# Kernel tuning notes

Measured on AMD Instinct MI355X. Metric: run time of the kernel, lower is better.

The kernel has to match this reference:

```python
import jax, jax.numpy as jnp
import numpy as np

D_IN = 1024
D_OUT = 1024
SEQ = 4096


def setup_inputs() -> dict:
    key = jax.random.key(0)
    kx, kq, kk, kv = jax.random.split(key, 4)
    s = 1.0 / np.sqrt(D_IN)
    return {
        "x": jax.random.normal(kx, (SEQ, D_IN), dtype=jnp.float32),
        # nn.Linear weights: shape [d_out, d_in], applied as x @ W.T
        "W_q": jax.random.uniform(kq, (D_OUT, D_IN), dtype=jnp.float32, minval=-s, maxval=s),
        "W_k": jax.random.uniform(kk, (D_OUT, D_IN), dtype=jnp.float32, minval=-s, maxval=s),
        "W_v": jax.random.uniform(kv, (D_OUT, D_IN), dtype=jnp.float32, minval=-s, maxval=s),
    }


def reference(x, W_q, W_k, W_v):
    # QKV projections (no bias)
    q = x @ W_q.T  # [N, d_out]
    k = x @ W_k.T
    v = x @ W_v.T
    d_k = k.shape[-1]
    scores = (q @ k.T) / jnp.sqrt(jnp.asarray(d_k, x.dtype))  # [N, N]
    attn = jax.nn.softmax(scores, axis=1)
    n = attn.shape[0]
    mask = jnp.tril(jnp.ones((n, n), dtype=attn.dtype))
    causal = attn * mask
    causal = causal / jnp.sum(causal, axis=1, keepdims=True)
    return causal @ v  # [N, d_out]
```

## Files before the change

kernel.cpp:

```cpp
#include <hip/hip_runtime.h>
#include <hip/hip_bf16.h>
#include <stdint.h>
#include <math.h>

#define SEQ 4096
#define DIM 1024

typedef __attribute__((ext_vector_type(8))) __bf16 bf16x8;
typedef __attribute__((ext_vector_type(4))) float f32x4;
typedef __attribute__((ext_vector_type(8))) unsigned short u16x8;

__device__ __forceinline__ unsigned short f2bf(float f) {
  unsigned int u = __float_as_uint(f);
  u = (u + 0x7FFFu + ((u >> 16) & 1u)) >> 16;
  return (unsigned short)u;
}

__device__ __forceinline__ int swz(int o) { return o ^ (((o >> 7) & 7) << 4); }

template <int N> __device__ __forceinline__ void wait_vm() {
  if constexpr (N == 0) asm volatile("s_waitcnt vmcnt(0)" ::: "memory");
  else if constexpr (N == 4) asm volatile("s_waitcnt vmcnt(4)" ::: "memory");
  else if constexpr (N == 6) asm volatile("s_waitcnt vmcnt(6)" ::: "memory");
  else if constexpr (N == 8) asm volatile("s_waitcnt vmcnt(8)" ::: "memory");
}

__global__ void __launch_bounds__(256) cvt_all(const float* __restrict__ x,
                                               const float* __restrict__ wq,
                                               const float* __restrict__ wk,
                                               const float* __restrict__ wv,
                                               unsigned short* __restrict__ xb,
                                               unsigned short* __restrict__ wqk,
                                               unsigned short* __restrict__ wvb) {
  const int bid = blockIdx.x;
  const float* src;
  unsigned short* dst;
  size_t base;
  if (bid < 2048)      { src = x;  dst = xb;                base = (size_t)bid * 2048; }
  else if (bid < 2560) { src = wq; dst = wqk;               base = (size_t)(bid - 2048) * 2048; }
  else if (bid < 3072) { src = wk; dst = wqk + 1024 * 1024; base = (size_t)(bid - 2560) * 2048; }
  else                 { src = wv; dst = wvb;               base = (size_t)(bid - 3072) * 2048; }
  size_t i = base + (size_t)threadIdx.x * 8;
  float4 a = *reinterpret_cast<const float4*>(src + i);
  float4 b = *reinterpret_cast<const float4*>(src + i + 4);
  u16x8 o;
  o[0] = f2bf(a.x); o[1] = f2bf(a.y); o[2] = f2bf(a.z); o[3] = f2bf(a.w);
  o[4] = f2bf(b.x); o[5] = f2bf(b.y); o[6] = f2bf(b.z); o[7] = f2bf(b.w);
  *reinterpret_cast<u16x8*>(dst + i) = o;
}

__global__ void __launch_bounds__(256) proj_qk(const unsigned short* __restrict__ A,
                                               const unsigned short* __restrict__ B,
                                               unsigned short* __restrict__ C) {
  constexpr int lda = DIM, ldb = DIM, ldc = 2048;
  const int tr = blockIdx.x >> 4, tc = blockIdx.x & 15;

  __shared__ __align__(16) unsigned short As[2][128 * 64];
  __shared__ __align__(16) unsigned short Bs[2][128 * 64];

  const int tid = threadIdx.x;
  const int lane = tid & 63;
  const int wid = tid >> 6;
  const int wr = wid >> 1, wc = wid & 1;
  const int l15 = lane & 15;
  const int kq = lane >> 4;

  f32x4 acc[4][4];
  #pragma unroll
  for (int m = 0; m < 4; ++m)
    #pragma unroll
    for (int n = 0; n < 4; ++n)
      acc[m][n] = (f32x4){0.f, 0.f, 0.f, 0.f};

  const unsigned short* Abase = A + (size_t)tr * 128 * lda;
  const unsigned short* Bbase = B + (size_t)tc * 128 * ldb;

  auto stage = [&](int buf, int kt) {
    const int k0 = kt << 6;
    #pragma unroll
    for (int i = 0; i < 4; ++i) {
      const int o = (i * 256 + tid) * 16;
      const int cs = (swz(o) >> 4) & 7;
      const unsigned short* ga = Abase + (size_t)(o >> 7) * lda + k0 + cs * 8;
      const unsigned short* gb = Bbase + (size_t)(o >> 7) * ldb + k0 + cs * 8;
      __builtin_amdgcn_global_load_lds(
          (const __attribute__((address_space(1))) unsigned int*)ga,
          (__attribute__((address_space(3))) unsigned int*)((char*)&As[buf][0] + o), 16, 0, 0);
      __builtin_amdgcn_global_load_lds(
          (const __attribute__((address_space(1))) unsigned int*)gb,
          (__attribute__((address_space(3))) unsigned int*)((char*)&Bs[buf][0] + o), 16, 0, 0);
    }
  };

  stage(0, 0);
  int cur = 0;
  for (int kt = 0; kt < 16; ++kt) {
    if (kt + 1 < 16) { stage(cur ^ 1, kt + 1); wait_vm<8>(); }
    else wait_vm<0>();
    __builtin_amdgcn_s_barrier();

    bf16x8 af[4][2], bv[4][2];
    #pragma unroll
    for (int m = 0; m < 4; ++m)
      #pragma unroll
      for (int ks = 0; ks < 2; ++ks) {
        const int row = wr * 64 + m * 16 + l15;
        af[m][ks] = *reinterpret_cast<const bf16x8*>(
            (const char*)&As[cur][0] + swz(row * 128 + kq * 16 + ks * 64));
      }
    #pragma unroll
    for (int n = 0; n < 4; ++n)
      #pragma unroll
      for (int ks = 0; ks < 2; ++ks) {
        const int row = wc * 64 + n * 16 + l15;
        bv[n][ks] = *reinterpret_cast<const bf16x8*>(
            (const char*)&Bs[cur][0] + swz(row * 128 + kq * 16 + ks * 64));
      }
    #pragma unroll
    for (int m = 0; m < 4; ++m)
      #pragma unroll
      for (int n = 0; n < 4; ++n) {
        acc[m][n] = __builtin_amdgcn_mfma_f32_16x16x32_bf16(af[m][0], bv[n][0], acc[m][n], 0, 0, 0);
        acc[m][n] = __builtin_amdgcn_mfma_f32_16x16x32_bf16(af[m][1], bv[n][1], acc[m][n], 0, 0, 0);
      }
    __builtin_amdgcn_s_barrier();
    cur ^= 1;
  }

  const int rbase = tr * 128 + wr * 64 + kq * 4;
  const int cbase = tc * 128 + wc * 64 + l15;
  #pragma unroll
  for (int m = 0; m < 4; ++m)
    #pragma unroll
    for (int n = 0; n < 4; ++n)
      #pragma unroll
      for (int i = 0; i < 4; ++i)
        C[(size_t)(rbase + m * 16 + i) * ldc + cbase + n * 16] = f2bf(acc[m][n][i]);
}

__global__ void __launch_bounds__(512) qkt_vt(const unsigned short* __restrict__ Q,
                                              const unsigned short* __restrict__ K,
                                              unsigned short* __restrict__ S,
                                              const unsigned short* __restrict__ wvb,
                                              const unsigned short* __restrict__ xb,
                                              unsigned short* __restrict__ vt) {
  __shared__ __align__(16) unsigned short As[2][256 * 64];
  __shared__ __align__(16) unsigned short Bs[2][256 * 64];

  const int bid = ((blockIdx.x & 7) << 5) + (blockIdx.x >> 3);
  const int tid = threadIdx.x;
  const int lane = tid & 63;
  const int wid = tid >> 6;

  if (bid < 136) {
    int tr = (int)((sqrtf(8.0f * bid + 1.0f) - 1.0f) * 0.5f);
    while ((tr + 1) * (tr + 2) / 2 <= bid) ++tr;
    while (tr * (tr + 1) / 2 > bid) --tr;
    const int tc = bid - tr * (tr + 1) / 2;

    constexpr int LDA = 2 * DIM, LDC = SEQ;
    constexpr float SCALE = 0.03125f;
    const int wr = wid >> 2;
    const int wc = wid & 3;
    const int l15 = lane & 15;
    const int kq = lane >> 4;

    const unsigned short* Abase = Q + (size_t)tr * 256 * LDA;
    const unsigned short* Bbase = K + (size_t)tc * 256 * LDA;

    f32x4 acc[8][4];
    #pragma unroll
    for (int m = 0; m < 8; ++m)
      #pragma unroll
      for (int n = 0; n < 4; ++n)
        acc[m][n] = (f32x4){0.f, 0.f, 0.f, 0.f};

    auto stage_half = [&](int buf, int kt, int h) {
      const int k0 = kt << 6;
      const bool isB = (h < 2);
      unsigned short* lb = isB ? &Bs[buf][0] : &As[buf][0];
      const unsigned short* gb = isB ? Bbase : Abase;
      #pragma unroll
      for (int i = 0; i < 2; ++i) {
        const int ot = ((h & 1) << 14) + ((i * 512 + tid) << 4);
        const int row = ot >> 7;
        const int cs = (swz(ot) >> 4) & 7;
        const unsigned short* g = gb + (size_t)row * LDA + k0 + cs * 8;
        __builtin_amdgcn_global_load_lds(
            (const __attribute__((address_space(1))) unsigned int*)g,
            (__attribute__((address_space(3))) unsigned int*)((char*)lb + ot), 16, 0, 0);
      }
    };

    bf16x8 a[4][2], bn0[2][2], bn1[2][2];

    auto rdA = [&](int b, int mi) {
      #pragma unroll
      for (int f = 0; f < 4; ++f) {
        const int row = wr * 128 + mi * 64 + f * 16 + l15;
        #pragma unroll
        for (int ks = 0; ks < 2; ++ks)
          a[f][ks] = *reinterpret_cast<const bf16x8*>(
              (const char*)&As[b][0] + swz(row * 128 + kq * 16 + ks * 64));
      }
    };
    auto rdB = [&](bf16x8 (&dst)[2][2], int b, int n) {
      #pragma unroll
      for (int g = 0; g < 2; ++g) {
        const int row = wc * 64 + n * 32 + g * 16 + l15;
        #pragma unroll
        for (int ks = 0; ks < 2; ++ks)
          dst[g][ks] = *reinterpret_cast<const bf16x8*>(
              (const char*)&Bs[b][0] + swz(row * 128 + kq * 16 + ks * 64));
      }
    };
    auto mma = [&](int mi, int n, bf16x8 (&bb)[2][2]) {
      #pragma unroll
      for (int f = 0; f < 4; ++f)
        #pragma unroll
        for (int g = 0; g < 2; ++g) {
          acc[mi * 4 + f][n * 2 + g] =
              __builtin_amdgcn_mfma_f32_16x16x32_bf16(a[f][0], bb[g][0], acc[mi * 4 + f][n * 2 + g], 0, 0, 0);
          acc[mi * 4 + f][n * 2 + g] =
              __builtin_amdgcn_mfma_f32_16x16x32_bf16(a[f][1], bb[g][1], acc[mi * 4 + f][n * 2 + g], 0, 0, 0);
        }
    };

    stage_half(0, 0, 0); stage_half(0, 0, 1); stage_half(0, 0, 2); stage_half(0, 0, 3);
    stage_half(1, 1, 0); stage_half(1, 1, 1);
    wait_vm<4>();
    __builtin_amdgcn_s_barrier();

    #pragma unroll 1
    for (int kt = 0; kt < 16; ++kt) {
      const int b = kt & 1;
      const bool pf1 = (kt + 1 < 16);
      const bool pf2 = (kt + 2 < 16);
      rdA(b, 0);
      rdB(bn0, b, 0);
      if (pf1) stage_half(b ^ 1, kt + 1, 2);
      __builtin_amdgcn_s_setprio(1); mma(0, 0, bn0); __builtin_amdgcn_s_setprio(0);
      __builtin_amdgcn_s_barrier();
      rdB(bn1, b, 1);
      if (pf1) stage_half(b ^ 1, kt + 1, 3);
      __builtin_amdgcn_s_setprio(1); mma(0, 1, bn1); __builtin_amdgcn_s_setprio(0);
      __builtin_amdgcn_s_barrier();
      rdA(b, 1);
      if (pf2) stage_half(b, kt + 2, 0);
      __builtin_amdgcn_s_setprio(1); mma(1, 1, bn1); __builtin_amdgcn_s_setprio(0);
      __builtin_amdgcn_s_barrier();
      if (pf2) stage_half(b, kt + 2, 1);
      if (pf1) { if (pf2) wait_vm<4>(); else wait_vm<0>(); }
      __builtin_amdgcn_s_setprio(1); mma(1, 0, bn0); __builtin_amdgcn_s_setprio(0);
      __builtin_amdgcn_s_barrier();
    }

    const int rb = tr * 256 + wr * 128 + kq * 4;
    const int cb = tc * 256 + wc * 64 + l15;
    #pragma unroll
    for (int am = 0; am < 8; ++am)
      #pragma unroll
      for (int an = 0; an < 4; ++an)
        #pragma unroll
        for (int i = 0; i < 4; ++i)
          S[(size_t)(rb + am * 16 + i) * LDC + cb + an * 16] = f2bf(acc[am][an][i] * SCALE);
    return;
  }

  const int wr = wid >> 1;
  const int wc = wid & 1;
  const int l15 = lane & 15;
  const int kq = lane >> 4;
  unsigned short* A0 = &As[0][0];
  unsigned short* B0 = &Bs[0][0];

  for (int t = bid - 136; t < 256; t += 120) {
    const int tr = t >> 5, tc = t & 31;
    const unsigned short* Abase = wvb + (size_t)tr * 128 * DIM;
    const unsigned short* Bbase = xb + (size_t)tc * 128 * DIM;

    f32x4 acc[2][4];
    #pragma unroll
    for (int m = 0; m < 2; ++m)
      #pragma unroll
      for (int n = 0; n < 4; ++n)
        acc[m][n] = (f32x4){0.f, 0.f, 0.f, 0.f};

    auto stage = [&](int buf, int kt) {
      const int k0 = kt << 6;
      #pragma unroll
      for (int i = 0; i < 2; ++i) {
        const int o = (i * 512 + tid) * 16;
        const int cs = (swz(o) >> 4) & 7;
        const unsigned short* ga = Abase + (size_t)(o >> 7) * DIM + k0 + cs * 8;
        const unsigned short* gb = Bbase + (size_t)(o >> 7) * DIM + k0 + cs * 8;
        __builtin_amdgcn_global_load_lds(
            (const __attribute__((address_space(1))) unsigned int*)ga,
            (__attribute__((address_space(3))) unsigned int*)((char*)(A0 + buf * 128 * 64) + o), 16, 0, 0);
        __builtin_amdgcn_global_load_lds(
            (const __attribute__((address_space(1))) unsigned int*)gb,
            (__attribute__((address_space(3))) unsigned int*)((char*)(B0 + buf * 128 * 64) + o), 16, 0, 0);
      }
    };

    stage(0, 0);
    int cur = 0;
    for (int kt = 0; kt < 16; ++kt) {
      if (kt + 1 < 16) { stage(cur ^ 1, kt + 1); wait_vm<4>(); }
      else wait_vm<0>();
      __builtin_amdgcn_s_barrier();

      bf16x8 af[2][2], bv[4][2];
      #pragma unroll
      for (int m = 0; m < 2; ++m)
        #pragma unroll
        for (int ks = 0; ks < 2; ++ks) {
          const int row = wr * 32 + m * 16 + l15;
          af[m][ks] = *reinterpret_cast<const bf16x8*>(
              (const char*)(A0 + cur * 128 * 64) + swz(row * 128 + kq * 16 + ks * 64));
        }
      #pragma unroll
      for (int n = 0; n < 4; ++n)
        #pragma unroll
        for (int ks = 0; ks < 2; ++ks) {
          const int row = wc * 64 + n * 16 + l15;
          bv[n][ks] = *reinterpret_cast<const bf16x8*>(
              (const char*)(B0 + cur * 128 * 64) + swz(row * 128 + kq * 16 + ks * 64));
        }
      #pragma unroll
      for (int m = 0; m < 2; ++m)
        #pragma unroll
        for (int n = 0; n < 4; ++n) {
          acc[m][n] = __builtin_amdgcn_mfma_f32_16x16x32_bf16(af[m][0], bv[n][0], acc[m][n], 0, 0, 0);
          acc[m][n] = __builtin_amdgcn_mfma_f32_16x16x32_bf16(af[m][1], bv[n][1], acc[m][n], 0, 0, 0);
        }
      __builtin_amdgcn_s_barrier();
      cur ^= 1;
    }

    const int rbase = tr * 128 + wr * 32 + kq * 4;
    const int cbase = tc * 128 + wc * 64 + l15;
    #pragma unroll
    for (int m = 0; m < 2; ++m)
      #pragma unroll
      for (int n = 0; n < 4; ++n)
        #pragma unroll
        for (int i = 0; i < 4; ++i)
          vt[(size_t)(rbase + m * 16 + i) * SEQ + cbase + n * 16] = f2bf(acc[m][n][i]);
    __builtin_amdgcn_s_barrier();
  }
}

__global__ void __launch_bounds__(256) pv_kernel(const unsigned short* __restrict__ A,
                                                 const unsigned short* __restrict__ B,
                                                 float* __restrict__ C,
                                                 float* __restrict__ P1, float* __restrict__ P2,
                                                 float* __restrict__ P3) {
  constexpr int BM = 64;
  constexpr int lda = SEQ, ldb = SEQ, ldc = DIM;
  int tc = blockIdx.x, tr = blockIdx.y;
  const int s = blockIdx.z;
  const int ltiles = tr + 1;
  int kt0 = s * 16;
  if (kt0 >= ltiles) return;
  const int nt = min(ltiles, kt0 + 16) - kt0;

  __shared__ __align__(16) unsigned short As[2][BM * 64];
  __shared__ __align__(16) unsigned short Bs[2][128 * 64];

  const int tid = threadIdx.x;
  const int lane = tid & 63;
  const int wid = tid >> 6;
  const int wr = wid >> 1, wc = wid & 1;
  const int l15 = lane & 15;
  const int kq = lane >> 4;

  f32x4 acc[2][4];
  #pragma unroll
  for (int m = 0; m < 2; ++m)
    #pragma unroll
    for (int n = 0; n < 4; ++n)
      acc[m][n] = (f32x4){0.f, 0.f, 0.f, 0.f};

  const unsigned short* Abase = A + (size_t)tr * BM * lda;
  const unsigned short* Bbase = B + (size_t)tc * 128 * ldb;

  auto stage = [&](int buf, int ktabs) {
    const int k0 = ktabs << 6;
    #pragma unroll
    for (int i = 0; i < 2; ++i) {
      const int o = (i * 256 + tid) * 16;
      const int cs = (swz(o) >> 4) & 7;
      const unsigned short* g = Abase + (size_t)(o >> 7) * lda + k0 + cs * 8;
      __builtin_amdgcn_global_load_lds(
          (const __attribute__((address_space(1))) unsigned int*)g,
          (__attribute__((address_space(3))) unsigned int*)((char*)&As[buf][0] + o), 16, 0, 0);
    }
    #pragma unroll
    for (int i = 0; i < 4; ++i) {
      const int o = (i * 256 + tid) * 16;
      const int cs = (swz(o) >> 4) & 7;
      const unsigned short* g = Bbase + (size_t)(o >> 7) * ldb + k0 + cs * 8;
      __builtin_amdgcn_global_load_lds(
          (const __attribute__((address_space(1))) unsigned int*)g,
          (__attribute__((address_space(3))) unsigned int*)((char*)&Bs[buf][0] + o), 16, 0, 0);
    }
  };

  stage(0, kt0);
  int cur = 0;
  for (int kt = 0; kt < nt; ++kt) {
    if (kt + 1 < nt) { stage(cur ^ 1, kt0 + kt + 1); wait_vm<6>(); }
    else wait_vm<0>();
    __builtin_amdgcn_s_barrier();

    bf16x8 af[2][2], bv[4][2];
    #pragma unroll
    for (int m = 0; m < 2; ++m)
      #pragma unroll
      for (int ks = 0; ks < 2; ++ks) {
        const int row = wr * 32 + m * 16 + l15;
        af[m][ks] = *reinterpret_cast<const bf16x8*>(
            (const char*)&As[cur][0] + swz(row * 128 + kq * 16 + ks * 64));
      }
    #pragma unroll
    for (int n = 0; n < 4; ++n)
      #pragma unroll
      for (int ks = 0; ks < 2; ++ks) {
        const int row = wc * 64 + n * 16 + l15;
        bv[n][ks] = *reinterpret_cast<const bf16x8*>(
            (const char*)&Bs[cur][0] + swz(row * 128 + kq * 16 + ks * 64));
      }
    #pragma unroll
    for (int m = 0; m < 2; ++m)
      #pragma unroll
      for (int n = 0; n < 4; ++n) {
        acc[m][n] = __builtin_amdgcn_mfma_f32_16x16x32_bf16(af[m][0], bv[n][0], acc[m][n], 0, 0, 0);
        acc[m][n] = __builtin_amdgcn_mfma_f32_16x16x32_bf16(af[m][1], bv[n][1], acc[m][n], 0, 0, 0);
      }
    __builtin_amdgcn_s_barrier();
    cur ^= 1;
  }

  float* fdst = C;
  int rowoff = 0;
  if (s == 1) { fdst = P1; rowoff = 1024; }
  else if (s == 2) { fdst = P2; rowoff = 2048; }
  else if (s == 3) { fdst = P3; rowoff = 3072; }
  const int rbase = tr * BM + wr * 32 + kq * 4;
  const int cbase = tc * 128 + wc * 64 + l15;
  #pragma unroll
  for (int m = 0; m < 2; ++m)
    #pragma unroll
    for (int n = 0; n < 4; ++n)
      #pragma unroll
      for (int i = 0; i < 4; ++i)
        fdst[(size_t)(rbase + m * 16 + i - rowoff) * ldc + cbase + n * 16] = acc[m][n][i];
}

__global__ void __launch_bounds__(256) reduce_kernel(float* __restrict__ out,
                                                     const float* __restrict__ p1,
                                                     const float* __restrict__ p2,
                                                     const float* __restrict__ p3) {
  const int b = blockIdx.x;
  const size_t e = ((size_t)b * 1024) + threadIdx.x * 4;
  f32x4 acc = *reinterpret_cast<f32x4*>(out + (size_t)1024 * 1024 + e);
  acc += *reinterpret_cast<const f32x4*>(p1 + e);
  if (b >= 1024) acc += *reinterpret_cast<const f32x4*>(p2 + e - (size_t)1024 * 1024);
  if (b >= 2048) acc += *reinterpret_cast<const f32x4*>(p3 + e - (size_t)2048 * 1024);
  *reinterpret_cast<f32x4*>(out + (size_t)1024 * 1024 + e) = acc;
}

__global__ void __launch_bounds__(512) softmax_causal2(unsigned short* __restrict__ S) {
  const int g = threadIdx.x >> 8;
  const int row = g ? (SEQ - 1 - blockIdx.x) : blockIdx.x;
  const int tid = threadIdx.x & 255;
  const int lane = threadIdx.x & 63;
  const int wid = (threadIdx.x >> 6) & 3;
  const int limit = ((row >> 6) + 1) << 6;
  unsigned short* Srow = S + (size_t)row * SEQ;

  float vals[16];
  bool act[2];
  #pragma unroll
  for (int i = 0; i < 2; ++i) {
    const int j0 = (tid + i * 256) * 8;
    act[i] = j0 < limit;
    if (act[i]) {
      const uint4 w = *reinterpret_cast<const uint4*>(Srow + j0);
      const unsigned int wb[4] = {w.x, w.y, w.z, w.w};
      #pragma unroll
      for (int e = 0; e < 4; ++e) {
        vals[i * 8 + 2 * e]     = __uint_as_float(wb[e] << 16);
        vals[i * 8 + 2 * e + 1] = __uint_as_float(wb[e] & 0xFFFF0000u);
      }
    } else {
      #pragma unroll
      for (int e = 0; e < 8; ++e) vals[i * 8 + e] = -1e30f;
    }
  }

  float m = -1e30f;
  #pragma unroll
  for (int i = 0; i < 2; ++i)
    #pragma unroll
    for (int e = 0; e < 8; ++e) {
      int j = (tid + i * 256) * 8 + e;
      if (j <= row) m = fmaxf(m, vals[i * 8 + e]);
    }
  #pragma unroll
  for (int off = 32; off > 0; off >>= 1) m = fmaxf(m, __shfl_xor(m, off));
  __shared__ float redm[2][4], reds[2][4];
  if (lane == 0) redm[g][wid] = m;
  __syncthreads();
  m = fmaxf(fmaxf(redm[g][0], redm[g][1]), fmaxf(redm[g][2], redm[g][3]));

  float s = 0.f;
  float ev[16];
  #pragma unroll
  for (int i = 0; i < 2; ++i)
    #pragma unroll
    for (int e = 0; e < 8; ++e) {
      int j = (tid + i * 256) * 8 + e;
      float ex = (j <= row) ? __expf(vals[i * 8 + e] - m) : 0.f;
      ev[i * 8 + e] = ex;
      s += ex;
    }
  #pragma unroll
  for (int off = 32; off > 0; off >>= 1) s += __shfl_xor(s, off);
  if (lane == 0) reds[g][wid] = s;
  __syncthreads();
  s = reds[g][0] + reds[g][1] + reds[g][2] + reds[g][3];
  const float inv = 1.f / s;

  #pragma unroll
  for (int i = 0; i < 2; ++i) {
    if (!act[i]) continue;
    u16x8 o;
    #pragma unroll
    for (int e = 0; e < 8; ++e) o[e] = f2bf(ev[i * 8 + e] * inv);
    *reinterpret_cast<u16x8*>(Srow + (tid + i * 256) * 8) = o;
  }
}

extern "C" void kernel_launch(void* const* d_in, const int* in_sizes, int n_in,
                              void* d_out, int out_size, void* d_ws, size_t ws_size,
                              hipStream_t stream) {
  const float* x  = (const float*)d_in[0];
  const float* Wq = (const float*)d_in[1];
  const float* Wk = (const float*)d_in[2];
  const float* Wv = (const float*)d_in[3];
  float* out = (float*)d_out;

  char* ws = (char*)d_ws;
  const size_t MB = 1u << 20;
  unsigned short* xb   = (unsigned short*)(ws + 0 * MB);
  unsigned short* wqk  = (unsigned short*)(ws + 8 * MB);
  unsigned short* wvb  = (unsigned short*)(ws + 12 * MB);
  unsigned short* qkb  = (unsigned short*)(ws + 14 * MB);
  unsigned short* vt   = (unsigned short*)(ws + 30 * MB);
  unsigned short* S    = (unsigned short*)(ws + 38 * MB);
  float* p1 = (float*)(ws + 0 * MB);
  float* p2 = (float*)(ws + 12 * MB);
  float* p3 = (float*)(ws + 20 * MB);

  cvt_all<<<3584, 256, 0, stream>>>(x, Wq, Wk, Wv, xb, wqk, wvb);

  proj_qk<<<512, 256, 0, stream>>>(xb, wqk, qkb);

  qkt_vt<<<256, 512, 0, stream>>>(qkb, qkb + 1024, S, wvb, xb, vt);

  softmax_causal2<<<SEQ / 2, 512, 0, stream>>>(S);

  pv_kernel<<<dim3(DIM / 128, SEQ / 64, 4), 256, 0, stream>>>(S, vt, out, p1, p2, p3);
  reduce_kernel<<<3072, 256, 0, stream>>>(out, p1, p2, p3);
}
```

Baseline: 124.6 us.

## Use 1024-thread blocks in QK^T/V^T kernel with simpler double-buffer loop

Doubles the block size of the fused QK^T and V^T kernel from 512 to 1024 threads, so each wave owns a 64x64 output tile instead of 128x64. The fine-grained four-phase interleaved staging and setprio schedule is replaced by a plain double-buffered loop with one prefetch per k-step. The V^T branch is re-tiled for 16 waves (2x2 fragments per wave, one load per operand). Smaller per-wave accumulators raise wave count per CU, but the new loop loses the finer compute/load overlap and 1024-thread blocks may limit scheduling.

```diff
diff --git a/kernel.cpp b/kernel.cpp
--- a/kernel.cpp
+++ b/kernel.cpp
@@ -20,6 +20,7 @@
 
 template <int N> __device__ __forceinline__ void wait_vm() {
   if constexpr (N == 0) asm volatile("s_waitcnt vmcnt(0)" ::: "memory");
+  else if constexpr (N == 2) asm volatile("s_waitcnt vmcnt(2)" ::: "memory");
   else if constexpr (N == 4) asm volatile("s_waitcnt vmcnt(4)" ::: "memory");
   else if constexpr (N == 6) asm volatile("s_waitcnt vmcnt(6)" ::: "memory");
   else if constexpr (N == 8) asm volatile("s_waitcnt vmcnt(8)" ::: "memory");
@@ -138,12 +139,12 @@
         C[(size_t)(rbase + m * 16 + i) * ldc + cbase + n * 16] = f2bf(acc[m][n][i]);
 }
 
-__global__ void __launch_bounds__(512) qkt_vt(const unsigned short* __restrict__ Q,
-                                              const unsigned short* __restrict__ K,
-                                              unsigned short* __restrict__ S,
-                                              const unsigned short* __restrict__ wvb,
-                                              const unsigned short* __restrict__ xb,
-                                              unsigned short* __restrict__ vt) {
+__global__ void __launch_bounds__(1024) qkt_vt(const unsigned short* __restrict__ Q,
+                                               const unsigned short* __restrict__ K,
+                                               unsigned short* __restrict__ S,
+                                               const unsigned short* __restrict__ wvb,
+                                               const unsigned short* __restrict__ xb,
+                                               unsigned short* __restrict__ vt) {
   __shared__ __align__(16) unsigned short As[2][256 * 64];
   __shared__ __align__(16) unsigned short Bs[2][256 * 64];
 
@@ -151,6 +152,10 @@
   const int tid = threadIdx.x;
   const int lane = tid & 63;
   const int wid = tid >> 6;
+  const int wr = wid >> 2;
+  const int wc = wid & 3;
+  const int l15 = lane & 15;
+  const int kq = lane >> 4;
 
   if (bid < 136) {
     int tr = (int)((sqrtf(8.0f * bid + 1.0f) - 1.0f) * 0.5f);
@@ -160,117 +165,82 @@
 
     constexpr int LDA = 2 * DIM, LDC = SEQ;
     constexpr float SCALE = 0.03125f;
-    const int wr = wid >> 2;
-    const int wc = wid & 3;
-    const int l15 = lane & 15;
-    const int kq = lane >> 4;
 
     const unsigned short* Abase = Q + (size_t)tr * 256 * LDA;
     const unsigned short* Bbase = K + (size_t)tc * 256 * LDA;
 
-    f32x4 acc[8][4];
-    #pragma unroll
-    for (int m = 0; m < 8; ++m)
+    f32x4 acc[4][4];
+    #pragma unroll
+    for (int m = 0; m < 4; ++m)
       #pragma unroll
       for (int n = 0; n < 4; ++n)
         acc[m][n] = (f32x4){0.f, 0.f, 0.f, 0.f};
 
-    auto stage_half = [&](int buf, int kt, int h) {
+    auto stage4 = [&](int buf, int kt) {
       const int k0 = kt << 6;
-      const bool isB = (h < 2);
-      unsigned short* lb = isB ? &Bs[buf][0] : &As[buf][0];
-      const unsigned short* gb = isB ? Bbase : Abase;
       #pragma unroll
       for (int i = 0; i < 2; ++i) {
-        const int ot = ((h & 1) << 14) + ((i * 512 + tid) << 4);
+        const int ot = (i * 1024 + tid) << 4;
         const int row = ot >> 7;
         const int cs = (swz(ot) >> 4) & 7;
-        const unsigned short* g = gb + (size_t)row * LDA + k0 + cs * 8;
+        const unsigned short* ga = Abase + (size_t)row * LDA + k0 + cs * 8;
+        const unsigned short* gb = Bbase + (size_t)row * LDA + k0 + cs * 8;
         __builtin_amdgcn_global_load_lds(
-            (const __attribute__((address_space(1))) unsigned int*)g,
-            (__attribute__((address_space(3))) unsigned int*)((char*)lb + ot), 16, 0, 0);
+            (const __attribute__((address_space(1))) unsigned int*)ga,
+            (__attribute__((address_space(3))) unsigned int*)((char*)&As[buf][0] + ot), 16, 0, 0);
+        __builtin_amdgcn_global_load_lds(
+            (const __attribute__((address_space(1))) unsigned int*)gb,
+            (__attribute__((address_space(3))) unsigned int*)((char*)&Bs[buf][0] + ot), 16, 0, 0);
       }
     };
 
-    bf16x8 a[4][2], bn0[2][2], bn1[2][2];
-
-    auto rdA = [&](int b, int mi) {
-      #pragma unroll
-      for (int f = 0; f < 4; ++f) {
-        const int row = wr * 128 + mi * 64 + f * 16 + l15;
-        #pragma unroll
-        for (int ks = 0; ks < 2; ++ks)
-          a[f][ks] = *reinterpret_cast<const bf16x8*>(
-              (const char*)&As[b][0] + swz(row * 128 + kq * 16 + ks * 64));
-      }
-    };
-    auto rdB = [&](bf16x8 (&dst)[2][2], int b, int n) {
-      #pragma unroll
-      for (int g = 0; g < 2; ++g) {
-        const int row = wc * 64 + n * 32 + g * 16 + l15;
-        #pragma unroll
-        for (int ks = 0; ks < 2; ++ks)
-          dst[g][ks] = *reinterpret_cast<const bf16x8*>(
-              (const char*)&Bs[b][0] + swz(row * 128 + kq * 16 + ks * 64));
-      }
-    };
-    auto mma = [&](int mi, int n, bf16x8 (&bb)[2][2]) {
-      #pragma unroll
-      for (int f = 0; f < 4; ++f)
-        #pragma unroll
-        for (int g = 0; g < 2; ++g) {
-          acc[mi * 4 + f][n * 2 + g] =
-              __builtin_amdgcn_mfma_f32_16x16x32_bf16(a[f][0], bb[g][0], acc[mi * 4 + f][n * 2 + g], 0, 0, 0);
-          acc[mi * 4 + f][n * 2 + g] =
-              __builtin_amdgcn_mfma_f32_16x16x32_bf16(a[f][1], bb[g][1], acc[mi * 4 + f][n * 2 + g], 0, 0, 0);
-        }
-    };
-
-    stage_half(0, 0, 0); stage_half(0, 0, 1); stage_half(0, 0, 2); stage_half(0, 0, 3);
-    stage_half(1, 1, 0); stage_half(1, 1, 1);
-    wait_vm<4>();
-    __builtin_amdgcn_s_barrier();
-
+    stage4(0, 0);
+    int cur = 0;
     #pragma unroll 1
     for (int kt = 0; kt < 16; ++kt) {
-      const int b = kt & 1;
-      const bool pf1 = (kt + 1 < 16);
-      const bool pf2 = (kt + 2 < 16);
-      rdA(b, 0);
-      rdB(bn0, b, 0);
-      if (pf1) stage_half(b ^ 1, kt + 1, 2);
-      __builtin_amdgcn_s_setprio(1); mma(0, 0, bn0); __builtin_amdgcn_s_setprio(0);
+      if (kt + 1 < 16) { stage4(cur ^ 1, kt + 1); wait_vm<4>(); }
+      else wait_vm<0>();
       __builtin_amdgcn_s_barrier();
-      rdB(bn1, b, 1);
-      if (pf1) stage_half(b ^ 1, kt + 1, 3);
-      __builtin_amdgcn_s_setprio(1); mma(0, 1, bn1); __builtin_amdgcn_s_setprio(0);
+
+      #pragma unroll
+      for (int ks = 0; ks < 2; ++ks) {
+        bf16x8 a[4], b[4];
+        #pragma unroll
+        for (int m = 0; m < 4; ++m) {
+          const int row = wr * 64 + m * 16 + l15;
+          a[m] = *reinterpret_cast<const bf16x8*>(
+              (const char*)&As[cur][0] + swz(row * 128 + kq * 16 + ks * 64));
+        }
+        #pragma unroll
+        for (int n = 0; n < 4; ++n) {
+          const int row = wc * 64 + n * 16 + l15;
+          b[n] = *reinterpret_cast<const bf16x8*>(
+              (const char*)&Bs[cur][0] + swz(row * 128 + kq * 16 + ks * 64));
+        }
+        __builtin_amdgcn_s_setprio(1);
+        #pragma unroll
+        for (int m = 0; m < 4; ++m)
+          #pragma unroll
+          for (int n = 0; n < 4; ++n)
+            acc[m][n] = __builtin_amdgcn_mfma_f32_16x16x32_bf16(a[m], b[n], acc[m][n], 0, 0, 0);
+        __builtin_amdgcn_s_setprio(0);
+      }
       __builtin_amdgcn_s_barrier();
-      rdA(b, 1);
-      if (pf2) stage_half(b, kt + 2, 0);
-      __builtin_amdgcn_s_setprio(1); mma(1, 1, bn1); __builtin_amdgcn_s_setprio(0);
-      __builtin_amdgcn_s_barrier();
-      if (pf2) stage_half(b, kt + 2, 1);
-      if (pf1) { if (pf2) wait_vm<4>(); else wait_vm<0>(); }
-      __builtin_amdgcn_s_setprio(1); mma(1, 0, bn0); __builtin_amdgcn_s_setprio(0);
-      __builtin_amdgcn_s_barrier();
-    }
-
-    const int rb = tr * 256 + wr * 128 + kq * 4;
+      cur ^= 1;
+    }
+
+    const int rb = tr * 256 + wr * 64 + kq * 4;
     const int cb = tc * 256 + wc * 64 + l15;
     #pragma unroll
-    for (int am = 0; am < 8; ++am)
-      #pragma unroll
-      for (int an = 0; an < 4; ++an)
+    for (int m = 0; m < 4; ++m)
+      #pragma unroll
+      for (int n = 0; n < 4; ++n)
         #pragma unroll
         for (int i = 0; i < 4; ++i)
-          S[(size_t)(rb + am * 16 + i) * LDC + cb + an * 16] = f2bf(acc[am][an][i] * SCALE);
+          S[(size_t)(rb + m * 16 + i) * LDC + cb + n * 16] = f2bf(acc[m][n][i] * SCALE);
     return;
   }
 
-  const int wr = wid >> 1;
-  const int wc = wid & 1;
-  const int l15 = lane & 15;
-  const int kq = lane >> 4;
   unsigned short* A0 = &As[0][0];
   unsigned short* B0 = &Bs[0][0];
 
@@ -279,38 +249,35 @@
     const unsigned short* Abase = wvb + (size_t)tr * 128 * DIM;
     const unsigned short* Bbase = xb + (size_t)tc * 128 * DIM;
 
-    f32x4 acc[2][4];
+    f32x4 acc[2][2];
     #pragma unroll
     for (int m = 0; m < 2; ++m)
       #pragma unroll
-      for (int n = 0; n < 4; ++n)
+      for (int n = 0; n < 2; ++n)
         acc[m][n] = (f32x4){0.f, 0.f, 0.f, 0.f};
 
     auto stage = [&](int buf, int kt) {
       const int k0 = kt << 6;
-      #pragma unroll
-      for (int i = 0; i < 2; ++i) {
-        const int o = (i * 512 + tid) * 16;
-        const int cs = (swz(o) >> 4) & 7;
-        const unsigned short* ga = Abase + (size_t)(o >> 7) * DIM + k0 + cs * 8;
-        const unsigned short* gb = Bbase + (size_t)(o >> 7) * DIM + k0 + cs * 8;
-        __builtin_amdgcn_global_load_lds(
-            (const __attribute__((address_space(1))) unsigned int*)ga,
-            (__attribute__((address_space(3))) unsigned int*)((char*)(A0 + buf * 128 * 64) + o), 16, 0, 0);
-        __builtin_amdgcn_global_load_lds(
-            (const __attribute__((address_space(1))) unsigned int*)gb,
-            (__attribute__((address_space(3))) unsigned int*)((char*)(B0 + buf * 128 * 64) + o), 16, 0, 0);
-      }
+      const int o = tid << 4;
+      const int cs = (swz(o) >> 4) & 7;
+      const unsigned short* ga = Abase + (size_t)(o >> 7) * DIM + k0 + cs * 8;
+      const unsigned short* gb = Bbase + (size_t)(o >> 7) * DIM + k0 + cs * 8;
+      __builtin_amdgcn_global_load_lds(
+          (const __attribute__((address_space(1))) unsigned int*)ga,
+          (__attribute__((address_space(3))) unsigned int*)((char*)(A0 + buf * 128 * 64) + o), 16, 0, 0);
+      __builtin_amdgcn_global_load_lds(
+          (const __attribute__((address_space(1))) unsigned int*)gb,
+          (__attribute__((address_space(3))) unsigned int*)((char*)(B0 + buf * 128 * 64) + o), 16, 0, 0);
     };
 
     stage(0, 0);
     int cur = 0;
     for (int kt = 0; kt < 16; ++kt) {
-      if (kt + 1 < 16) { stage(cur ^ 1, kt + 1); wait_vm<4>(); }
+      if (kt + 1 < 16) { stage(cur ^ 1, kt + 1); wait_vm<2>(); }
       else wait_vm<0>();
       __builtin_amdgcn_s_barrier();
 
-      bf16x8 af[2][2], bv[4][2];
+      bf16x8 af[2][2], bv[2][2];
       #pragma unroll
       for (int m = 0; m < 2; ++m)
         #pragma unroll
@@ -320,17 +287,17 @@
               (const char*)(A0 + cur * 128 * 64) + swz(row * 128 + kq * 16 + ks * 64));
         }
       #pragma unroll
-      for (int n = 0; n < 4; ++n)
+      for (int n = 0; n < 2; ++n)
         #pragma unroll
         for (int ks = 0; ks < 2; ++ks) {
-          const int row = wc * 64 + n * 16 + l15;
+          const int row = wc * 32 + n * 16 + l15;
           bv[n][ks] = *reinterpret_cast<const bf16x8*>(
               (const char*)(B0 + cur * 128 * 64) + swz(row * 128 + kq * 16 + ks * 64));
         }
       #pragma unroll
       for (int m = 0; m < 2; ++m)
         #pragma unroll
-        for (int n = 0; n < 4; ++n) {
+        for (int n = 0; n < 2; ++n) {
           acc[m][n] = __builtin_amdgcn_mfma_f32_16x16x32_bf16(af[m][0], bv[n][0], acc[m][n], 0, 0, 0);
           acc[m][n] = __builtin_amdgcn_mfma_f32_16x16x32_bf16(af[m][1], bv[n][1], acc[m][n], 0, 0, 0);
         }
@@ -339,11 +306,11 @@
     }
 
     const int rbase = tr * 128 + wr * 32 + kq * 4;
-    const int cbase = tc * 128 + wc * 64 + l15;
+    const int cbase = tc * 128 + wc * 32 + l15;
     #pragma unroll
     for (int m = 0; m < 2; ++m)
       #pragma unroll
-      for (int n = 0; n < 4; ++n)
+      for (int n = 0; n < 2; ++n)
         #pragma unroll
         for (int i = 0; i < 4; ++i)
           vt[(size_t)(rbase + m * 16 + i) * SEQ + cbase + n * 16] = f2bf(acc[m][n][i]);
@@ -568,7 +535,7 @@
 
   proj_qk<<<512, 256, 0, stream>>>(xb, wqk, qkb);
 
-  qkt_vt<<<256, 512, 0, stream>>>(qkb, qkb + 1024, S, wvb, xb, vt);
+  qkt_vt<<<256, 1024, 0, stream>>>(qkb, qkb + 1024, S, wvb, xb, vt);
 
   softmax_causal2<<<SEQ / 2, 512, 0, stream>>>(S);
 
```

Result: no change. 125.6 us (+0.8%).
